# Optimization experiments

Hardware: AMD Instinct MI355X
Metric: run time of the kernel (lower is better)

The kernel has to match this reference:

```python
import jax, jax.numpy as jnp
import numpy as np

ATOM_FDIM = 133
BOND_FDIM = 147
HIDDEN = 300
DEPTH = 3
N_ATOMS = 100000
N_BONDS = 200000
MAX_NB = 6
N_MOLS = 4000


def setup_inputs() -> dict:
    key = jax.random.key(0)
    ks = jax.random.split(key, 10)
    f_atoms = jax.random.normal(ks[0], (N_ATOMS, ATOM_FDIM), dtype=jnp.float32)
    f_bonds = jax.random.normal(ks[1], (N_BONDS, BOND_FDIM), dtype=jnp.float32)
    a2b = jax.random.randint(ks[2], (N_ATOMS, MAX_NB), 0, N_BONDS)
    b2a = jax.random.randint(ks[3], (N_BONDS,), 0, N_ATOMS)
    b2revb = jax.random.randint(ks[4], (N_BONDS,), 0, N_BONDS)
    atom2mol = jnp.sort(jax.random.randint(ks[5], (N_ATOMS,), 0, N_MOLS))
    s = 1.0 / np.sqrt(HIDDEN)
    W_i = jax.random.uniform(ks[6], (BOND_FDIM, HIDDEN), jnp.float32, -s, s)
    W_h = jax.random.uniform(ks[7], (HIDDEN, HIDDEN), jnp.float32, -s, s)
    W_o_w = jax.random.uniform(ks[8], (ATOM_FDIM + HIDDEN, HIDDEN), jnp.float32, -s, s)
    W_o_b = jax.random.uniform(ks[9], (HIDDEN,), jnp.float32, -s, s)
    return {"f_atoms": f_atoms, "f_bonds": f_bonds, "a2b": a2b, "b2a": b2a,
            "b2revb": b2revb, "atom2mol": atom2mol, "W_i": W_i, "W_h": W_h,
            "W_o_w": W_o_w, "W_o_b": W_o_b}


def reference(f_atoms, f_bonds, a2b, b2a, b2revb, atom2mol, W_i, W_h, W_o_w, W_o_b):
    # input = W_i(f_bonds); message = act(input)
    inp = f_bonds @ W_i                      # [n_bonds, hidden]
    message = jax.nn.relu(inp)
    for _ in range(DEPTH - 1):
        # gather neighbor bond messages per atom and sum: [n_atoms, max_nb, h] -> [n_atoms, h]
        a_message = message[a2b].sum(axis=1)
        rev_message = message[b2revb]        # [n_bonds, hidden]
        message = a_message[b2a] - rev_message
        message = jax.nn.relu(inp + message @ W_h)
    # final atom-level aggregation
    a_message = message[a2b].sum(axis=1)     # [n_atoms, hidden]
    a_input = jnp.concatenate([f_atoms, a_message], axis=1)
    atom_hiddens = jax.nn.relu(a_input @ W_o_w + W_o_b)
    # segment mean pooling over molecules
    sums = jax.ops.segment_sum(atom_hiddens, atom2mol, num_segments=N_MOLS)
    counts = jax.ops.segment_sum(jnp.ones((atom_hiddens.shape[0],), atom_hiddens.dtype),
                                 atom2mol, num_segments=N_MOLS)
    mol_vecs = sums / jnp.maximum(counts, 1.0)[:, None]  # zero vec for empty mols
    return mol_vecs
```

## Files before the change

### kernel.cpp

```cpp
#include <hip/hip_runtime.h>
#include <stdint.h>

#define ATOM_FDIM 133
#define BOND_FDIM 147
#define HIDDEN    300
#define N_ATOMS   100000
#define N_BONDS   200000
#define MAX_NB    6
#define N_MOLS    4000

#define KP_I 160
#define KP_H 320
#define KP_O 448
#define LDA  304
#define CPR  38

#define TM   128
#define NPAD 384
#define ACH  8
#define BCH  24

typedef unsigned short u16;
typedef short bf16x8 __attribute__((ext_vector_type(8)));
typedef float f32x4 __attribute__((ext_vector_type(4)));

__device__ __forceinline__ u16 f2bu(float f) {
    unsigned u = __float_as_uint(f);
    u += 0x7FFFu + ((u >> 16) & 1u);
    return (u16)(u >> 16);
}
__device__ __forceinline__ float bu2f(u16 b) { return __uint_as_float(((unsigned)b) << 16); }

#define AS1 __attribute__((address_space(1)))
#define AS3 __attribute__((address_space(3)))
__device__ __forceinline__ void gl_lds16(const void* g, void* l) {
    __builtin_amdgcn_global_load_lds((const AS1 void*)g, (AS3 void*)l, 16, 0, 0);
}

template <int EPI>
__global__ __launch_bounds__(512, 2) void mm_k(
    const u16* __restrict__ A, int lda,
    const u16* __restrict__ Wp,
    const float* __restrict__ bias,
    u16* __restrict__ out0, int ldo0,
    u16* __restrict__ out1, int ldo1,
    int M, int NT)
{
    __shared__ __align__(16) u16 As[2][ACH * 512];
    __shared__ __align__(16) u16 Bs[2][BCH * 512];

    const int t    = threadIdx.x;
    const int lane = t & 63, wid = t >> 6;
    const int fl   = lane & 15, fh = lane >> 4;
    const int m0   = blockIdx.x * TM;
    const int wr   = wid >> 1, wc = wid & 1;

    int arow = m0 + wid * 16 + fl;
    if (arow > M - 1) arow = M - 1;
    const size_t srcA = (size_t)arow * (size_t)lda * 2u + (size_t)(fh * 16);
    const size_t srcB = (size_t)(3 * wid) * 1024u + (size_t)lane * 16u;

    char* ldsA_of[2] = { (char*)As[0] + wid * 1024, (char*)As[1] + wid * 1024 };
    char* ldsB_of[2] = { (char*)Bs[0] + 3 * wid * 1024, (char*)Bs[1] + 3 * wid * 1024 };

    f32x4 acc[2][12] = {};

    gl_lds16((const char*)A + srcA, ldsA_of[0]);
    #pragma unroll
    for (int j = 0; j < 3; ++j)
        gl_lds16((const char*)Wp + srcB + (size_t)j * 1024, ldsB_of[0] + j * 1024);
    asm volatile("s_waitcnt vmcnt(0)" ::: "memory");
    __builtin_amdgcn_s_barrier();

    int cur = 0;
    for (int tt = 0; tt < NT; ++tt) {
        const int nxt = cur ^ 1;
        int w1 = tt + 1; if (w1 >= NT) w1 = 0;
        const u16* as_c = As[cur];
        const u16* bs_c = Bs[cur];
        const size_t kbA = (size_t)w1 * 64u;
        const size_t kbB = (size_t)w1 * (BCH * 1024u);

        gl_lds16((const char*)A + srcA + kbA, ldsA_of[nxt]);
        #pragma unroll
        for (int j = 0; j < 3; ++j)
            gl_lds16((const char*)Wp + kbB + srcB + (size_t)j * 1024,
                     ldsB_of[nxt] + j * 1024);

        bf16x8 af0, af1, bfv[12];
        af0 = *reinterpret_cast<const bf16x8*>(&as_c[(wr * 2 + 0) * 512 + lane * 8]);
        af1 = *reinterpret_cast<const bf16x8*>(&as_c[(wr * 2 + 1) * 512 + lane * 8]);
        #pragma unroll
        for (int n = 0; n < 6; ++n)
            bfv[n] = *reinterpret_cast<const bf16x8*>(&bs_c[(wc * 12 + n) * 512 + lane * 8]);
        __builtin_amdgcn_s_barrier();
        __builtin_amdgcn_s_setprio(1);
        #pragma unroll
        for (int n = 0; n < 6; ++n) {
            acc[0][n] = __builtin_amdgcn_mfma_f32_16x16x32_bf16(af0, bfv[n], acc[0][n], 0, 0, 0);
            acc[1][n] = __builtin_amdgcn_mfma_f32_16x16x32_bf16(af1, bfv[n], acc[1][n], 0, 0, 0);
        }
        __builtin_amdgcn_s_setprio(0);
        __builtin_amdgcn_s_barrier();

        #pragma unroll
        for (int n = 6; n < 12; ++n)
            bfv[n] = *reinterpret_cast<const bf16x8*>(&bs_c[(wc * 12 + n) * 512 + lane * 8]);
        __builtin_amdgcn_s_setprio(1);
        #pragma unroll
        for (int n = 6; n < 12; ++n) {
            acc[0][n] = __builtin_amdgcn_mfma_f32_16x16x32_bf16(af0, bfv[n], acc[0][n], 0, 0, 0);
            acc[1][n] = __builtin_amdgcn_mfma_f32_16x16x32_bf16(af1, bfv[n], acc[1][n], 0, 0, 0);
        }
        __builtin_amdgcn_s_setprio(0);
        asm volatile("s_waitcnt vmcnt(0)" ::: "memory");
        __builtin_amdgcn_s_barrier();

        cur = nxt;
    }

    #pragma unroll
    for (int m = 0; m < 2; ++m) {
        #pragma unroll
        for (int r = 0; r < 4; ++r) {
            const int row = m0 + wr * 32 + m * 16 + fh * 4 + r;
            if (row >= M) continue;
            #pragma unroll
            for (int n = 0; n < 12; ++n) {
                const int col = wc * 192 + n * 16 + fl;
                if (col >= HIDDEN) continue;
                const float v = acc[m][n][r];
                if (EPI == 0) {
                    out0[(size_t)row * ldo0 + col] = f2bu(v);
                    out1[(size_t)row * ldo1 + col] = f2bu(fmaxf(v, 0.f));
                } else if (EPI == 1) {
                    out0[(size_t)row * ldo0 + col] = f2bu(v);
                } else {
                    out0[(size_t)row * ldo0 + col] = f2bu(fmaxf(v + bias[col], 0.f));
                }
            }
        }
    }
}

__global__ __launch_bounds__(256) void wconv_k(const float* __restrict__ W, int Ks, int NT,
                                               u16* __restrict__ Wp)
{
    const int id = blockIdx.x * 256 + threadIdx.x;
    if (id >= NT * BCH * 512) return;
    const int block = id >> 9, rem = id & 511;
    const int l = rem >> 3, e = rem & 7;
    const int c = block % BCH, kt = block / BCH;
    const int col = c * 16 + (l & 15);
    const int k   = kt * 32 + (l >> 4) * 8 + e;
    const float v = (col < HIDDEN && k < Ks) ? W[(size_t)k * HIDDEN + col] : 0.f;
    Wp[id] = f2bu(v);
}

__global__ __launch_bounds__(256) void fbconv_k(const float* __restrict__ fb, u16* __restrict__ dst)
{
    const int id = blockIdx.x * 256 + threadIdx.x;
    if (id >= N_BONDS * KP_I) return;
    const int r = id / KP_I, k = id - r * KP_I;
    dst[id] = f2bu(k < BOND_FDIM ? fb[(size_t)r * BOND_FDIM + k] : 0.f);
}

__global__ __launch_bounds__(256) void agg_k(const u16* __restrict__ src,
                                             const int* __restrict__ a2b,
                                             u16* __restrict__ dst)
{
    const int c = blockIdx.x * 256 + threadIdx.x;
    if (c >= N_ATOMS * CPR) return;
    const int a = c / CPR, q = c - a * CPR;
    const int h = q * 8;
    const int* nb = a2b + (size_t)a * MAX_NB;
    float s[8] = {};
    #pragma unroll
    for (int j = 0; j < MAX_NB; ++j) {
        const int r = nb[j];
        union { uint4 u; u16 s[8]; } x;
        x.u = *(const uint4*)(src + (size_t)r * LDA + h);
        #pragma unroll
        for (int e = 0; e < 8; ++e) s[e] += bu2f(x.s[e]);
    }
    union { uint4 u; u16 s[8]; } o;
    #pragma unroll
    for (int e = 0; e < 8; ++e) o.s[e] = f2bu(s[e]);
    *(uint4*)(dst + (size_t)a * LDA + h) = o.u;
}

__global__ __launch_bounds__(256) void comb_k(const u16* __restrict__ inp,
                                              const u16* __restrict__ aY,
                                              const u16* __restrict__ Y,
                                              const int* __restrict__ b2a,
                                              const int* __restrict__ b2revb,
                                              u16* __restrict__ msg)
{
    const int c = blockIdx.x * 256 + threadIdx.x;
    if (c >= N_BONDS * CPR) return;
    const int b = c / CPR, q = c - b * CPR;
    const int h = q * 8;
    const int ia = b2a[b], ir = b2revb[b];
    union { uint4 u; u16 s[8]; } xi, xa, xy, o;
    xi.u = *(const uint4*)(inp + (size_t)b * LDA + h);
    xa.u = *(const uint4*)(aY + (size_t)ia * LDA + h);
    xy.u = *(const uint4*)(Y + (size_t)ir * LDA + h);
    #pragma unroll
    for (int j = 0; j < 8; ++j)
        o.s[j] = f2bu(fmaxf(bu2f(xi.s[j]) + bu2f(xa.s[j]) - bu2f(xy.s[j]), 0.f));
    *(uint4*)(msg + (size_t)b * LDA + h) = o.u;
}

__global__ __launch_bounds__(256) void concat_k(const float* __restrict__ fa,
                                                const u16* __restrict__ amsg,
                                                u16* __restrict__ dst)
{
    const int id = blockIdx.x * 256 + threadIdx.x;
    if (id >= N_ATOMS * KP_O) return;
    const int a = id / KP_O, k = id - a * KP_O;
    float v;
    if (k < ATOM_FDIM)                 v = fa[(size_t)a * ATOM_FDIM + k];
    else if (k < ATOM_FDIM + HIDDEN)   v = bu2f(amsg[(size_t)a * LDA + (k - ATOM_FDIM)]);
    else                               v = 0.f;
    dst[id] = f2bu(v);
}

__global__ __launch_bounds__(320) void pool_k(const u16* __restrict__ ah,
                                              const int* __restrict__ a2m,
                                              float* __restrict__ out)
{
    const int m = blockIdx.x;
    int lo, hi;
    { int l = 0, r = N_ATOMS;
      while (l < r) { int mid = (l + r) >> 1; if (a2m[mid] < m) l = mid + 1; else r = mid; }
      lo = l; }
    { int l = lo, r = N_ATOMS;
      while (l < r) { int mid = (l + r) >> 1; if (a2m[mid] < m + 1) l = mid + 1; else r = mid; }
      hi = l; }
    const float inv = 1.0f / (float)((hi - lo) > 1 ? (hi - lo) : 1);
    const int h = threadIdx.x;
    if (h >= HIDDEN) return;
    float s = 0.f;
    for (int a = lo; a < hi; ++a) s += bu2f(ah[(size_t)a * LDA + h]);
    out[(size_t)m * HIDDEN + h] = s * inv;
}

extern "C" void kernel_launch(void* const* d_in, const int* in_sizes, int n_in,
                              void* d_out, int out_size, void* d_ws, size_t ws_size,
                              hipStream_t stream)
{
    const float* f_atoms  = (const float*)d_in[0];
    const float* f_bonds  = (const float*)d_in[1];
    const int*   a2b      = (const int*)d_in[2];
    const int*   b2a      = (const int*)d_in[3];
    const int*   b2revb   = (const int*)d_in[4];
    const int*   atom2mol = (const int*)d_in[5];
    const float* W_i      = (const float*)d_in[6];
    const float* W_h      = (const float*)d_in[7];
    const float* W_o_w    = (const float*)d_in[8];
    const float* W_o_b    = (const float*)d_in[9];
    float* out = (float*)d_out;

    char* p = (char*)d_ws;
    auto alloc = [&](size_t bytes) { char* r = p; p += (bytes + 255) & ~(size_t)255; return r; };
    u16* inp = (u16*)alloc(((size_t)N_BONDS + 16) * LDA * 2);
    u16* msg = (u16*)alloc(((size_t)N_BONDS + 16) * LDA * 2);
    u16* Yb  = (u16*)alloc(((size_t)N_BONDS + 16) * LDA * 2);
    u16* aY  = (u16*)alloc(((size_t)N_ATOMS + 16) * LDA * 2);
    u16* Wpi = (u16*)alloc((size_t)(KP_I / 32) * BCH * 512 * 2);
    u16* Wph = (u16*)alloc((size_t)(KP_H / 32) * BCH * 512 * 2);
    u16* Wpo = (u16*)alloc((size_t)(KP_O / 32) * BCH * 512 * 2);
    if ((size_t)(p - (char*)d_ws) > ws_size) return;

    u16* fb16   = Yb;
    u16* concat = Yb;
    u16* ah     = msg;

    const dim3 blk(256);
    auto g1 = [](long long n) { return dim3((unsigned)((n + 255) / 256)); };
    const dim3 blk5(512);
    const dim3 gB((N_BONDS + TM - 1) / TM);
    const dim3 gA((N_ATOMS + TM - 1) / TM);

    wconv_k<<<g1((long long)(KP_I / 32) * BCH * 512), blk, 0, stream>>>(W_i, BOND_FDIM, KP_I / 32, Wpi);
    wconv_k<<<g1((long long)(KP_H / 32) * BCH * 512), blk, 0, stream>>>(W_h, HIDDEN, KP_H / 32, Wph);
    wconv_k<<<g1((long long)(KP_O / 32) * BCH * 512), blk, 0, stream>>>(W_o_w, ATOM_FDIM + HIDDEN, KP_O / 32, Wpo);
    fbconv_k<<<g1((long long)N_BONDS * KP_I), blk, 0, stream>>>(f_bonds, fb16);

    mm_k<0><<<gB, blk5, 0, stream>>>(fb16, KP_I, Wpi, nullptr,
                                     inp, LDA, msg, LDA, N_BONDS, KP_I / 32);

    for (int it = 0; it < 2; ++it) {
        mm_k<1><<<gB, blk5, 0, stream>>>(msg, LDA, Wph, nullptr,
                                         Yb, LDA, nullptr, 0, N_BONDS, KP_H / 32);
        agg_k<<<g1((long long)N_ATOMS * CPR), blk, 0, stream>>>(Yb, a2b, aY);
        comb_k<<<g1((long long)N_BONDS * CPR), blk, 0, stream>>>(inp, aY, Yb, b2a, b2revb, msg);
    }

    agg_k<<<g1((long long)N_ATOMS * CPR), blk, 0, stream>>>(msg, a2b, aY);
    concat_k<<<g1((long long)N_ATOMS * KP_O), blk, 0, stream>>>(f_atoms, aY, concat);
    mm_k<2><<<gA, blk5, 0, stream>>>(concat, KP_O, Wpo, W_o_b,
                                     ah, LDA, nullptr, 0, N_ATOMS, KP_O / 32);
    pool_k<<<dim3(N_MOLS), dim3(320), 0, stream>>>(ah, atom2mol, out);
}
```

Measured before the change: 1.022 ms.

## Deepen GEMM LDS pipeline to four stages and fuse final aggregation with concat

After: 950.7 us. 1.07x faster.

```diff
diff --git a/kernel.cpp b/kernel.cpp
--- a/kernel.cpp
+++ b/kernel.cpp
@@ -16,7 +16,6 @@
 #define CPR  38
 
 #define TM   128
-#define NPAD 384
 #define ACH  8
 #define BCH  24
 
@@ -46,8 +45,8 @@
     u16* __restrict__ out1, int ldo1,
     int M, int NT)
 {
-    __shared__ __align__(16) u16 As[2][ACH * 512];
-    __shared__ __align__(16) u16 Bs[2][BCH * 512];
+    __shared__ __align__(16) u16 As[4 * ACH * 512];
+    __shared__ __align__(16) u16 Bs[4 * BCH * 512];
 
     const int t    = threadIdx.x;
     const int lane = t & 63, wid = t >> 6;
@@ -60,64 +59,57 @@
     const size_t srcA = (size_t)arow * (size_t)lda * 2u + (size_t)(fh * 16);
     const size_t srcB = (size_t)(3 * wid) * 1024u + (size_t)lane * 16u;
 
-    char* ldsA_of[2] = { (char*)As[0] + wid * 1024, (char*)As[1] + wid * 1024 };
-    char* ldsB_of[2] = { (char*)Bs[0] + 3 * wid * 1024, (char*)Bs[1] + 3 * wid * 1024 };
+    char* ldsAbase = (char*)As + wid * 1024;
+    char* ldsBbase = (char*)Bs + 3 * wid * 1024;
+
+#define STAGE(buf, kt) do {                                               \
+        const size_t kbA_ = (size_t)(kt) * 64u;                           \
+        const size_t kbB_ = (size_t)(kt) * (size_t)(BCH * 1024);          \
+        char* la_ = ldsAbase + (size_t)(buf) * (ACH * 1024);              \
+        char* lb_ = ldsBbase + (size_t)(buf) * (BCH * 1024);              \
+        gl_lds16((const char*)A + srcA + kbA_, la_);                      \
+        gl_lds16((const char*)Wp + kbB_ + srcB,        lb_);              \
+        gl_lds16((const char*)Wp + kbB_ + srcB + 1024, lb_ + 1024);       \
+        gl_lds16((const char*)Wp + kbB_ + srcB + 2048, lb_ + 2048);       \
+    } while (0)
 
     f32x4 acc[2][12] = {};
 
-    gl_lds16((const char*)A + srcA, ldsA_of[0]);
-    #pragma unroll
-    for (int j = 0; j < 3; ++j)
-        gl_lds16((const char*)Wp + srcB + (size_t)j * 1024, ldsB_of[0] + j * 1024);
-    asm volatile("s_waitcnt vmcnt(0)" ::: "memory");
+    STAGE(0, 0);
+    STAGE(1, 1);
+    STAGE(2, 2);
+    asm volatile("s_waitcnt vmcnt(8)" ::: "memory");
     __builtin_amdgcn_s_barrier();
 
     int cur = 0;
     for (int tt = 0; tt < NT; ++tt) {
-        const int nxt = cur ^ 1;
-        int w1 = tt + 1; if (w1 >= NT) w1 = 0;
-        const u16* as_c = As[cur];
-        const u16* bs_c = Bs[cur];
-        const size_t kbA = (size_t)w1 * 64u;
-        const size_t kbB = (size_t)w1 * (BCH * 1024u);
-
-        gl_lds16((const char*)A + srcA + kbA, ldsA_of[nxt]);
-        #pragma unroll
-        for (int j = 0; j < 3; ++j)
-            gl_lds16((const char*)Wp + kbB + srcB + (size_t)j * 1024,
-                     ldsB_of[nxt] + j * 1024);
-
+        int w3 = tt + 3; if (w3 >= NT) w3 -= NT;
+        const int nx3 = (cur + 3) & 3;
+        STAGE(nx3, w3);
+
+        const u16* as_c = As + cur * (ACH * 512);
+        const u16* bs_c = Bs + cur * (BCH * 512);
         bf16x8 af0, af1, bfv[12];
         af0 = *reinterpret_cast<const bf16x8*>(&as_c[(wr * 2 + 0) * 512 + lane * 8]);
         af1 = *reinterpret_cast<const bf16x8*>(&as_c[(wr * 2 + 1) * 512 + lane * 8]);
         #pragma unroll
-        for (int n = 0; n < 6; ++n)
+        for (int n = 0; n < 12; ++n)
             bfv[n] = *reinterpret_cast<const bf16x8*>(&bs_c[(wc * 12 + n) * 512 + lane * 8]);
-        __builtin_amdgcn_s_barrier();
+
         __builtin_amdgcn_s_setprio(1);
         #pragma unroll
-        for (int n = 0; n < 6; ++n) {
+        for (int n = 0; n < 12; ++n) {
             acc[0][n] = __builtin_amdgcn_mfma_f32_16x16x32_bf16(af0, bfv[n], acc[0][n], 0, 0, 0);
             acc[1][n] = __builtin_amdgcn_mfma_f32_16x16x32_bf16(af1, bfv[n], acc[1][n], 0, 0, 0);
         }
         __builtin_amdgcn_s_setprio(0);
+
+        asm volatile("s_waitcnt vmcnt(8)" ::: "memory");
         __builtin_amdgcn_s_barrier();
 
-        #pragma unroll
-        for (int n = 6; n < 12; ++n)
-            bfv[n] = *reinterpret_cast<const bf16x8*>(&bs_c[(wc * 12 + n) * 512 + lane * 8]);
-        __builtin_amdgcn_s_setprio(1);
-        #pragma unroll
-        for (int n = 6; n < 12; ++n) {
-            acc[0][n] = __builtin_amdgcn_mfma_f32_16x16x32_bf16(af0, bfv[n], acc[0][n], 0, 0, 0);
-            acc[1][n] = __builtin_amdgcn_mfma_f32_16x16x32_bf16(af1, bfv[n], acc[1][n], 0, 0, 0);
-        }
-        __builtin_amdgcn_s_setprio(0);
-        asm volatile("s_waitcnt vmcnt(0)" ::: "memory");
-        __builtin_amdgcn_s_barrier();
-
-        cur = nxt;
-    }
+        cur = (cur + 1) & 3;
+    }
+#undef STAGE
 
     #pragma unroll
     for (int m = 0; m < 2; ++m) {
@@ -143,7 +135,8 @@
     }
 }
 
-__global__ __launch_bounds__(256) void wconv_k(const float* __restrict__ W, int Ks, int NT,
+__global__ __launch_bounds__(256) void wconv_k(const float* __restrict__ W,
+                                               int split, int off1, int Ktot, int NT,
                                                u16* __restrict__ Wp)
 {
     const int id = blockIdx.x * 256 + threadIdx.x;
@@ -153,7 +146,16 @@
     const int c = block % BCH, kt = block / BCH;
     const int col = c * 16 + (l & 15);
     const int k   = kt * 32 + (l >> 4) * 8 + e;
-    const float v = (col < HIDDEN && k < Ks) ? W[(size_t)k * HIDDEN + col] : 0.f;
+    float v = 0.f;
+    if (col < HIDDEN) {
+        if (k < split) {
+            const int r = k + off1;
+            if (r < Ktot) v = W[(size_t)r * HIDDEN + col];
+        } else {
+            const int r = k - split;
+            if (r < off1) v = W[(size_t)r * HIDDEN + col];
+        }
+    }
     Wp[id] = f2bu(v);
 }
 
@@ -211,18 +213,34 @@
     *(uint4*)(msg + (size_t)b * LDA + h) = o.u;
 }
 
-__global__ __launch_bounds__(256) void concat_k(const float* __restrict__ fa,
-                                                const u16* __restrict__ amsg,
+__global__ __launch_bounds__(256) void aggcat_k(const u16* __restrict__ msg,
+                                                const int* __restrict__ a2b,
+                                                const float* __restrict__ fa,
                                                 u16* __restrict__ dst)
 {
     const int id = blockIdx.x * 256 + threadIdx.x;
-    if (id >= N_ATOMS * KP_O) return;
-    const int a = id / KP_O, k = id - a * KP_O;
-    float v;
-    if (k < ATOM_FDIM)                 v = fa[(size_t)a * ATOM_FDIM + k];
-    else if (k < ATOM_FDIM + HIDDEN)   v = bu2f(amsg[(size_t)a * LDA + (k - ATOM_FDIM)]);
-    else                               v = 0.f;
-    dst[id] = f2bu(v);
+    if (id >= N_ATOMS * (KP_O / 4)) return;
+    const int a = id / (KP_O / 4), c = id - a * (KP_O / 4);
+    const int e0 = c * 4;
+    union { uint2 u; u16 s[4]; } o;
+    if (e0 < HIDDEN) {
+        const int* nb = a2b + (size_t)a * MAX_NB;
+        float s0 = 0.f, s1 = 0.f, s2 = 0.f, s3 = 0.f;
+        #pragma unroll
+        for (int j = 0; j < MAX_NB; ++j) {
+            union { uint2 u; u16 s[4]; } x;
+            x.u = *(const uint2*)(msg + (size_t)nb[j] * LDA + e0);
+            s0 += bu2f(x.s[0]); s1 += bu2f(x.s[1]); s2 += bu2f(x.s[2]); s3 += bu2f(x.s[3]);
+        }
+        o.s[0] = f2bu(s0); o.s[1] = f2bu(s1); o.s[2] = f2bu(s2); o.s[3] = f2bu(s3);
+    } else {
+        #pragma unroll
+        for (int j = 0; j < 4; ++j) {
+            const int fi = e0 + j - HIDDEN;
+            o.s[j] = (fi < ATOM_FDIM) ? f2bu(fa[(size_t)a * ATOM_FDIM + fi]) : (u16)0;
+        }
+    }
+    *(uint2*)(dst + (size_t)a * KP_O + e0) = o.u;
 }
 
 __global__ __launch_bounds__(320) void pool_k(const u16* __restrict__ ah,
@@ -282,9 +300,13 @@
     const dim3 gB((N_BONDS + TM - 1) / TM);
     const dim3 gA((N_ATOMS + TM - 1) / TM);
 
-    wconv_k<<<g1((long long)(KP_I / 32) * BCH * 512), blk, 0, stream>>>(W_i, BOND_FDIM, KP_I / 32, Wpi);
-    wconv_k<<<g1((long long)(KP_H / 32) * BCH * 512), blk, 0, stream>>>(W_h, HIDDEN, KP_H / 32, Wph);
-    wconv_k<<<g1((long long)(KP_O / 32) * BCH * 512), blk, 0, stream>>>(W_o_w, ATOM_FDIM + HIDDEN, KP_O / 32, Wpo);
+    const int BIGSPLIT = 1 << 20;
+    wconv_k<<<g1((long long)(KP_I / 32) * BCH * 512), blk, 0, stream>>>(
+        W_i, BIGSPLIT, 0, BOND_FDIM, KP_I / 32, Wpi);
+    wconv_k<<<g1((long long)(KP_H / 32) * BCH * 512), blk, 0, stream>>>(
+        W_h, BIGSPLIT, 0, HIDDEN, KP_H / 32, Wph);
+    wconv_k<<<g1((long long)(KP_O / 32) * BCH * 512), blk, 0, stream>>>(
+        W_o_w, HIDDEN, ATOM_FDIM, ATOM_FDIM + HIDDEN, KP_O / 32, Wpo);
     fbconv_k<<<g1((long long)N_BONDS * KP_I), blk, 0, stream>>>(f_bonds, fb16);
 
     mm_k<0><<<gB, blk5, 0, stream>>>(fb16, KP_I, Wpi, nullptr,
@@ -297,8 +319,7 @@
         comb_k<<<g1((long long)N_BONDS * CPR), blk, 0, stream>>>(inp, aY, Yb, b2a, b2revb, msg);
     }
 
-    agg_k<<<g1((long long)N_ATOMS * CPR), blk, 0, stream>>>(msg, a2b, aY);
-    concat_k<<<g1((long long)N_ATOMS * KP_O), blk, 0, stream>>>(f_atoms, aY, concat);
+    aggcat_k<<<g1((long long)N_ATOMS * (KP_O / 4)), blk, 0, stream>>>(msg, a2b, f_atoms, concat);
     mm_k<2><<<gA, blk5, 0, stream>>>(concat, KP_O, Wpo, W_o_b,
                                      ah, LDA, nullptr, 0, N_ATOMS, KP_O / 32);
     pool_k<<<dim3(N_MOLS), dim3(320), 0, stream>>>(ah, atom2mol, out);
```
